# Kernel tuning notes

Hardware: AMD Instinct MI355X
Metric: run time of the kernel (lower is better)

## Reference

```python
import jax, jax.numpy as jnp
import numpy as np

WS = 10                      # window radius
K = 2 * WS + 1               # 21
K2 = K * K                   # 441 window positions
SIG_COLOR = 1.0 / (0.1 * 0.1 * 2.0)
SIG_SPACE = 1.0 / (7.0 * 7.0 * 2.0)
LP = 0.8
C1 = 10.0
C2 = 5.0
ALPHA = 5.0
EPS = 1e-6


def _patches(img):
    """torch nn.Unfold(kernel_size=image_size, padding=WS) trick: returns the
    K2 zero-padded shifted copies of the image, shape (b, K2, c, h, w)."""
    b, c, h, w = img.shape
    p = jax.lax.conv_general_dilated_patches(img, (K, K), (1, 1), [(WS, WS), (WS, WS)])
    # (b, c*K2, h, w) with channel-major (c, ky, kx) ordering -> (b, K2, c, h, w)
    return p.reshape(b, c, K2, h, w).transpose(0, 2, 1, 3, 4)


def _edge_response(img):
    # local contrast: sum over window and channels of |I_j - I_i| (zero-padded
    # / non-positive neighbors masked out), shape (b, h, w)
    p = _patches(img)
    d = jnp.where(p > 0, p - img[:, None], 0.0)
    return jnp.abs(d).sum(axis=(1, 2))


def setup_inputs() -> dict:
    key = jax.random.key(0)
    k1, k2 = jax.random.split(key)
    original_images = jax.random.uniform(k1, (1, 3, 224, 224), dtype=jnp.float32)
    smooth_images = jax.random.uniform(k2, (1, 3, 224, 224), dtype=jnp.float32)
    return {"original_images": original_images, "smooth_images": smooth_images}


def reference(original_images, smooth_images):
    b, c, h, w = smooth_images.shape

    # ti_minus_tj: |T_j - T_i| with zero/non-positive padded neighbors zeroed;
    # the shifted copies are detached in the original (stop_gradient)
    sp = jax.lax.stop_gradient(_patches(smooth_images))
    ti = jnp.abs(jnp.where(sp > 0, sp - smooth_images[:, None], 0.0))  # (b,K2,c,h,w)

    # edge-response based region masks
    er_o = _edge_response(original_images)
    er_s = _edge_response(smooth_images)
    use_large = ((er_o < C1) & (er_s - er_o > C2))[:, None, None]  # (b,1,1,h,w)

    # spatial affinity ws (constant gaussian over window offsets)
    dy = jnp.arange(-WS, WS + 1)
    ws = jnp.exp(-SIG_SPACE * (dy[:, None] ** 2 + dy[None, :] ** 2).astype(jnp.float32))
    ws = ws.reshape(1, K2, 1, 1, 1)

    # color affinity wr from the guidance (original) image; note the original
    # code computes the affinity BEFORE masking the color difference, so the
    # affinity includes zero-padded neighbors -- replicated faithfully
    op = jax.lax.stop_gradient(_patches(original_images))
    cd = ((op - original_images[:, None]) ** 2).sum(axis=2, keepdims=True)  # (b,K2,1,h,w)
    wr = jnp.exp(-SIG_COLOR * cd)

    ws = jnp.where(use_large, ws, 0.0)
    wr = jnp.where(~use_large, wr, 0.0)

    scale = 1.0 / (h * w * b) / (WS * WS)  # note: window_size**2, not K2 (quirk kept)
    return scale * jnp.sum(ALPHA * ws * ti ** 2 + wr * (ti + EPS) ** LP)
```

## Files before the change

kernel.cpp:

```cpp
#include <hip/hip_runtime.h>


#define WSR 10
#define KK  21
#define HH  224
#define WW  224
#define HWSZ (HH*WW)
#define SIG_COLOR 50.0f
#define LPW 0.8f
#define C1T 10.0f
#define C2T 5.0f
#define ALPHA_W 5.0f
#define EPSV 1e-6f
#define LOG2E 1.44269504088896f
#define NSC (-SIG_COLOR * LOG2E)
#define SSP ((1.0f/98.0f) * LOG2E)

#define TX 64
#define TY 2
#define HALO_W (TX + 2*WSR)
#define HALO_H (TY + 2*WSR)
#define HSZ (HALO_W * HALO_H)
#define NBX 4
#define NBY (HH / TY)
#define NBLK (NBX * NBY)
#define SCALEF (1.0f / ((float)HWSZ * 100.0f))

__device__ __forceinline__ float fexp2(float x) { return __builtin_amdgcn_exp2f(x); }
__device__ __forceinline__ float flog2(float x) { return __builtin_amdgcn_logf(x); }

static constexpr float WXT[KK] = {
  0.3604486f, 0.4375650f, 0.5204496f, 0.6065307f, 0.6925675f,
  0.7748383f, 0.8493658f, 0.9122539f, 0.9600054f, 0.9898479f,
  1.0f,
  0.9898479f, 0.9600054f, 0.9122539f, 0.8493658f, 0.7748383f,
  0.6925675f, 0.6065307f, 0.5204496f, 0.4375650f, 0.3604486f };

__global__ __launch_bounds__(512) void smooth_loss_fused(
    const float* __restrict__ orig, const float* __restrict__ smo,
    float* __restrict__ out)
{
    __shared__ float2 tA[HSZ];
    __shared__ float2 tB[HSZ];
    __shared__ float2 tC[HSZ];
    __shared__ float racc0[512], racc1[512], racc2[512], racc3[512];
    __shared__ float red[2];

    const int tid = threadIdx.x;
    const int bid = blockIdx.x;
    const int bx  = bid & (NBX - 1);
    const int by  = bid >> 2;

    const int gx0 = bx * TX - WSR;
    const int gy0 = by * TY - WSR;
    for (int i = tid; i < HSZ; i += 512) {
        int r = i / HALO_W;
        int c = i - r * HALO_W;
        int gy = gy0 + r, gx = gx0 + c;
        bool v = ((unsigned)gy < (unsigned)HH) & ((unsigned)gx < (unsigned)WW);
        int gi = gy * WW + gx;
        float o0=0.f,o1=0.f,o2=0.f,s0=0.f,s1=0.f,s2=0.f;
        if (v) {
            o0 = orig[gi]; o1 = orig[gi+HWSZ]; o2 = orig[gi+2*HWSZ];
            s0 = smo[gi];  s1 = smo[gi+HWSZ];  s2 = smo[gi+2*HWSZ];
        }
        tA[i] = make_float2(o0,o1);
        tB[i] = make_float2(o2,s0);
        tC[i] = make_float2(s1,s2);
    }
    __syncthreads();

    const int lane = tid & 63;
    const int wv   = tid >> 6;
    const int prow = wv & 1;
    const int kg   = wv >> 1;

    const int cpos = (prow + WSR) * HALO_W + (lane + WSR);
    const float2 cA = tA[cpos], cB = tB[cpos], cC = tC[cpos];
    const float oc0=cA.x, oc1=cA.y, oc2=cB.x, sc0=cB.y, sc1=cC.x, sc2=cC.y;

    float er_o=0.f, er_s=0.f, sl=0.f, ss=0.f;

    const int nrows = (kg == 0) ? 6 : 5;
    int ky = kg;
    for (int i = 0; i < nrows; ++i, ky += 4) {
        const float dy = (float)(ky - WSR);
        const float wy = fexp2(-SSP * dy * dy);
        const float2* __restrict__ rA = &tA[(prow + ky) * HALO_W + lane];
        const float2* __restrict__ rB = &tB[(prow + ky) * HALO_W + lane];
        const float2* __restrict__ rC = &tC[(prow + ky) * HALO_W + lane];
        float srow = 0.f;
        #pragma unroll
        for (int kx = 0; kx < KK; ++kx) {
            float2 A = rA[kx];
            float2 B = rB[kx];
            float2 C = rC[kx];
            float e0 = A.x - oc0, e1 = A.y - oc1, e2 = B.x - oc2;
            float a0 = (A.x > 0.f) ? fabsf(e0) : 0.f;
            float a1 = (A.y > 0.f) ? fabsf(e1) : 0.f;
            float a2 = (B.x > 0.f) ? fabsf(e2) : 0.f;
            er_o += (a0 + a1) + a2;
            float t0 = (B.y > 0.f) ? fabsf(B.y - sc0) : 0.f;
            float t1 = (C.x > 0.f) ? fabsf(C.x - sc1) : 0.f;
            float t2 = (C.y > 0.f) ? fabsf(C.y - sc2) : 0.f;
            er_s += (t0 + t1) + t2;
            float cd = fmaf(e0, e0, fmaf(e1, e1, e2*e2));
            float wr = fexp2(NSC * cd);
            float tt = fmaf(t0, t0, fmaf(t1, t1, t2*t2));
            srow = fmaf(WXT[kx], tt, srow);
            float p0 = fexp2(LPW * flog2(t0 + EPSV));
            float p1 = fexp2(LPW * flog2(t1 + EPSV));
            float p2 = fexp2(LPW * flog2(t2 + EPSV));
            ss = fmaf(wr, (p0 + p1) + p2, ss);
        }
        sl = fmaf(wy, srow, sl);
    }

    racc0[tid]=er_o; racc1[tid]=er_s; racc2[tid]=sl; racc3[tid]=ss;
    __syncthreads();

    if (tid < 128) {
        float eo=0.f, es=0.f, l=0.f, s=0.f;
        #pragma unroll
        for (int k = 0; k < 4; ++k) {
            int t2i = lane + 64 * (prow + 2*k);
            eo += racc0[t2i]; es += racc1[t2i];
            l  += racc2[t2i]; s  += racc3[t2i];
        }
        bool use_large = (eo < C1T) && ((es - eo) > C2T);
        float contrib = use_large ? (ALPHA_W * l) : s;
        int px = bx * TX + lane;
        if (px >= WW) contrib = 0.f;
        #pragma unroll
        for (int off = 32; off > 0; off >>= 1)
            contrib += __shfl_down(contrib, off, 64);
        if (lane == 0) red[wv] = contrib;
    }
    __syncthreads();

    if (tid == 0)
        atomicAdd(out, (red[0] + red[1]) * SCALEF);
}

extern "C" void kernel_launch(void* const* d_in, const int* in_sizes, int n_in,
                              void* d_out, int out_size, void* d_ws, size_t ws_size,
                              hipStream_t stream) {
    const float* orig = (const float*)d_in[0];
    const float* smo  = (const float*)d_in[1];
    float* out = (float*)d_out;

    hipMemsetAsync(d_out, 0, sizeof(float), stream);
    smooth_loss_fused<<<NBLK, 512, 0, stream>>>(orig, smo, out);
}
```

Measured before the change: 101.3 us.

## Process one output row per block with eight wavefronts splitting window rows

Each block now handles a single image row, and its eight wavefronts split the 21 window rows among themselves, so the grid doubles to 896 blocks. The final reduction drops a barrier and issues the atomic straight from wave 0. Shared-memory loads are software-prefetched one column ahead, and launch bounds now request 6 waves per SIMD. The aim is more blocks for better load balance across CUs and shorter per-thread serial chains. The cost is more halo reloading per output pixel (21 rows loaded for 1 output row instead of 22 for 2), twice as many atomics, and possible register pressure from the occupancy hint.

```diff
diff --git a/kernel.cpp b/kernel.cpp
--- a/kernel.cpp
+++ b/kernel.cpp
@@ -17,13 +17,11 @@
 #define SSP ((1.0f/98.0f) * LOG2E)
 
 #define TX 64
-#define TY 2
 #define HALO_W (TX + 2*WSR)
-#define HALO_H (TY + 2*WSR)
+#define HALO_H (1 + 2*WSR)
 #define HSZ (HALO_W * HALO_H)
 #define NBX 4
-#define NBY (HH / TY)
-#define NBLK (NBX * NBY)
+#define NBLK (NBX * HH)
 #define SCALEF (1.0f / ((float)HWSZ * 100.0f))
 
 __device__ __forceinline__ float fexp2(float x) { return __builtin_amdgcn_exp2f(x); }
@@ -36,7 +34,7 @@
   0.9898479f, 0.9600054f, 0.9122539f, 0.8493658f, 0.7748383f,
   0.6925675f, 0.6065307f, 0.5204496f, 0.4375650f, 0.3604486f };
 
-__global__ __launch_bounds__(512) void smooth_loss_fused(
+__global__ __launch_bounds__(512, 6) void smooth_loss_fused(
     const float* __restrict__ orig, const float* __restrict__ smo,
     float* __restrict__ out)
 {
@@ -44,7 +42,6 @@
     __shared__ float2 tB[HSZ];
     __shared__ float2 tC[HSZ];
     __shared__ float racc0[512], racc1[512], racc2[512], racc3[512];
-    __shared__ float red[2];
 
     const int tid = threadIdx.x;
     const int bid = blockIdx.x;
@@ -52,7 +49,7 @@
     const int by  = bid >> 2;
 
     const int gx0 = bx * TX - WSR;
-    const int gy0 = by * TY - WSR;
+    const int gy0 = by - WSR;
     for (int i = tid; i < HSZ; i += 512) {
         int r = i / HALO_W;
         int c = i - r * HALO_W;
@@ -62,7 +59,7 @@
         float o0=0.f,o1=0.f,o2=0.f,s0=0.f,s1=0.f,s2=0.f;
         if (v) {
             o0 = orig[gi]; o1 = orig[gi+HWSZ]; o2 = orig[gi+2*HWSZ];
-            s0 = smo[gi];  s1 = smo[gi+HWSZ];  s2 = smo[gi+2*HWSZ];
+            s0 = smo[gi];  s1 = smo[gi+HWSZ]; s2 = smo[gi+2*HWSZ];
         }
         tA[i] = make_float2(o0,o1);
         tB[i] = make_float2(o2,s0);
@@ -71,30 +68,28 @@
     __syncthreads();
 
     const int lane = tid & 63;
-    const int wv   = tid >> 6;
-    const int prow = wv & 1;
-    const int kg   = wv >> 1;
+    const int kg   = tid >> 6;
 
-    const int cpos = (prow + WSR) * HALO_W + (lane + WSR);
+    const int cpos = WSR * HALO_W + (lane + WSR);
     const float2 cA = tA[cpos], cB = tB[cpos], cC = tC[cpos];
     const float oc0=cA.x, oc1=cA.y, oc2=cB.x, sc0=cB.y, sc1=cC.x, sc2=cC.y;
 
     float er_o=0.f, er_s=0.f, sl=0.f, ss=0.f;
 
-    const int nrows = (kg == 0) ? 6 : 5;
+    const int nrows = (kg < 5) ? 3 : 2;
     int ky = kg;
-    for (int i = 0; i < nrows; ++i, ky += 4) {
-        const float dy = (float)(ky - WSR);
-        const float wy = fexp2(-SSP * dy * dy);
-        const float2* __restrict__ rA = &tA[(prow + ky) * HALO_W + lane];
-        const float2* __restrict__ rB = &tB[(prow + ky) * HALO_W + lane];
-        const float2* __restrict__ rC = &tC[(prow + ky) * HALO_W + lane];
+    for (int i = 0; i < nrows; ++i, ky += 8) {
+        const float dyf = (float)(ky - WSR);
+        const float wy = fexp2(-SSP * dyf * dyf);
+        const float2* __restrict__ rA = &tA[ky * HALO_W + lane];
+        const float2* __restrict__ rB = &tB[ky * HALO_W + lane];
+        const float2* __restrict__ rC = &tC[ky * HALO_W + lane];
         float srow = 0.f;
+        float2 A = rA[0], B = rB[0], C = rC[0];
         #pragma unroll
         for (int kx = 0; kx < KK; ++kx) {
-            float2 A = rA[kx];
-            float2 B = rB[kx];
-            float2 C = rC[kx];
+            float2 A1 = A, B1 = B, C1 = C;
+            if (kx < KK-1) { A1 = rA[kx+1]; B1 = rB[kx+1]; C1 = rC[kx+1]; }
             float e0 = A.x - oc0, e1 = A.y - oc1, e2 = B.x - oc2;
             float a0 = (A.x > 0.f) ? fabsf(e0) : 0.f;
             float a1 = (A.y > 0.f) ? fabsf(e1) : 0.f;
@@ -112,6 +107,7 @@
             float p1 = fexp2(LPW * flog2(t1 + EPSV));
             float p2 = fexp2(LPW * flog2(t2 + EPSV));
             ss = fmaf(wr, (p0 + p1) + p2, ss);
+            A = A1; B = B1; C = C1;
         }
         sl = fmaf(wy, srow, sl);
     }
@@ -119,27 +115,24 @@
     racc0[tid]=er_o; racc1[tid]=er_s; racc2[tid]=sl; racc3[tid]=ss;
     __syncthreads();
 
-    if (tid < 128) {
+    if (tid < 64) {
         float eo=0.f, es=0.f, l=0.f, s=0.f;
         #pragma unroll
-        for (int k = 0; k < 4; ++k) {
-            int t2i = lane + 64 * (prow + 2*k);
-            eo += racc0[t2i]; es += racc1[t2i];
-            l  += racc2[t2i]; s  += racc3[t2i];
+        for (int k = 0; k < 8; ++k) {
+            int idx = tid + 64 * k;
+            eo += racc0[idx]; es += racc1[idx];
+            l  += racc2[idx]; s  += racc3[idx];
         }
         bool use_large = (eo < C1T) && ((es - eo) > C2T);
         float contrib = use_large ? (ALPHA_W * l) : s;
-        int px = bx * TX + lane;
+        int px = bx * TX + tid;
         if (px >= WW) contrib = 0.f;
         #pragma unroll
         for (int off = 32; off > 0; off >>= 1)
             contrib += __shfl_down(contrib, off, 64);
-        if (lane == 0) red[wv] = contrib;
+        if (tid == 0)
+            atomicAdd(out, contrib * SCALEF);
     }
-    __syncthreads();
-
-    if (tid == 0)
-        atomicAdd(out, (red[0] + red[1]) * SCALEF);
 }
 
 extern "C" void kernel_launch(void* const* d_in, const int* in_sizes, int n_in,
```

After: 119.2 us. 1.18x slower.
